# Kernel optimization log

Measured on AMD Instinct MI355X. Metric: run time of the kernel, lower is better.

The kernel has to match this reference:

```python
import jax, jax.numpy as jnp
import numpy as np

B, T, C, HS = 8, 2048, 1024, 64
SCALE = C ** (-0.5)  # NOTE: source scales by C, not head_size
NEG_INF = float('-inf')
NEG_BIG = -1e9


def setup_inputs() -> dict:
    key = jax.random.key(0)
    kV, kK, kQ, kWq, kWk, kWv, kL = jax.random.split(key, 7)
    V = jax.random.normal(kV, (B, T, C), dtype=jnp.float32)
    K = jax.random.normal(kK, (B, T, C), dtype=jnp.float32)
    Q = jax.random.normal(kQ, (B, T, C), dtype=jnp.float32)
    w_scale = 1.0 / np.sqrt(C)
    Wq = jax.random.normal(kWq, (C, HS), dtype=jnp.float32) * w_scale
    Wk = jax.random.normal(kWk, (C, HS), dtype=jnp.float32) * w_scale
    Wv = jax.random.normal(kWv, (C, HS), dtype=jnp.float32) * w_scale
    # padding only at the tail; valid lengths in [T//2, T] so no NaN softmax rows
    lengths = jax.random.randint(kL, (B,), T // 2, T + 1)
    pad_mask = (jnp.arange(T)[None, None, :] >= lengths[:, None, None])  # [B,1,T] bool
    return {"V": V, "K": K, "Q": Q, "Wq": Wq, "Wk": Wk, "Wv": Wv, "pad_mask": pad_mask}


def reference(V, K, Q, Wq, Wk, Wv, pad_mask):
    q = Q @ Wq  # [B,T,HS]
    k = K @ Wk
    v = V @ Wv
    A = jnp.einsum('btd,bsd->bts', q, k) * SCALE  # [B,T,T]
    t = A.shape[1]
    causal = jnp.triu(jnp.ones((t, A.shape[2]), dtype=bool), k=1)  # tril==0
    A = jnp.where(causal[None], NEG_INF, A)
    A = jnp.where(pad_mask, NEG_INF, A)  # mask padded key columns
    A = jnp.where(jnp.swapaxes(pad_mask, -2, -1)[:, :t, :], NEG_BIG, A)  # padded query rows
    A = jax.nn.softmax(A, axis=-1)
    return A @ v  # [B,T,HS]
```

## Files before the change

kernel.cpp:

```cpp
#include <hip/hip_runtime.h>
#include <hip/hip_bf16.h>

typedef short bf16x8 __attribute__((ext_vector_type(8)));
typedef float f32x4 __attribute__((ext_vector_type(4)));
typedef unsigned int u32;
typedef u32 u32x4 __attribute__((ext_vector_type(4)));

#define T_SEQ 2048
#define NB 8
#define NEGB (-1e30f)

__device__ inline unsigned short f2bf(float f) {
  unsigned u = __builtin_bit_cast(unsigned, f);
  u += 0x7FFFu + ((u >> 16) & 1u);
  return (unsigned short)(u >> 16);
}
__device__ inline float bf2f(unsigned short h) {
  unsigned u = ((unsigned)h) << 16;
  return __builtin_bit_cast(float, u);
}
__device__ inline u32 cvt2(float a, float b) {
  __hip_bfloat162 h = __float22bfloat162_rn(make_float2(a, b));
  u32 r;
  __builtin_memcpy(&r, &h, 4);
  return r;
}
__device__ inline bf16x8 pack8(float4 a, float4 b) {
  u32x4 p;
  p[0] = cvt2(a.x, a.y);
  p[1] = cvt2(a.z, a.w);
  p[2] = cvt2(b.x, b.y);
  p[3] = cvt2(b.z, b.w);
  return __builtin_bit_cast(bf16x8, p);
}
__device__ inline f32x4 mfma16(bf16x8 a, bf16x8 b, f32x4 c) {
  return __builtin_amdgcn_mfma_f32_16x16x32_bf16(a, b, c, 0, 0, 0);
}
__device__ __forceinline__ void gl_lds16(const void* g, void* l) {
  __builtin_amdgcn_global_load_lds(
      (const __attribute__((address_space(1))) void*)g,
      (__attribute__((address_space(3))) void*)l, 16, 0, 0);
}

__global__ void detect_k(const unsigned char* m, int* flag) {
  __shared__ int ones, bad;
  int tid = threadIdx.x;
  if (tid == 0) { ones = 0; bad = 0; }
  __syncthreads();
  int lo = 0, lb = 0;
  for (int i = tid; i < NB * T_SEQ; i += 256) {
    int v = (m[i] != 0);
    lo += v;
    if (i & 3) lb += v;
  }
  atomicAdd(&ones, lo);
  atomicAdd(&bad, lb);
  __syncthreads();
  if (tid == 0) *flag = (ones > 0 && bad == 0) ? 1 : 0;
}

__global__ void lengths_k(const unsigned char* m, const int* flag, int* lengths) {
  int b = blockIdx.x, tid = threadIdx.x;
  int cnt = 0;
  if (*flag) {
    const int* mi = (const int*)m;
    for (int t = tid; t < T_SEQ; t += 256) cnt += (mi[b * T_SEQ + t] == 0);
  } else {
    for (int t = tid; t < T_SEQ; t += 256) cnt += (m[b * T_SEQ + t] == 0);
  }
  for (int off = 32; off >= 1; off >>= 1) cnt += __shfl_xor(cnt, off);
  __shared__ int wsum[4];
  if ((tid & 63) == 0) wsum[tid >> 6] = cnt;
  __syncthreads();
  if (tid == 0) lengths[b] = wsum[0] + wsum[1] + wsum[2] + wsum[3];
}

__global__ void wt_k(const float* Wq, const float* Wk, const float* Wv,
                     unsigned short* wt) {
  int e = blockIdx.x * 256 + threadIdx.x;
  if (e >= 3 * 64 * 1024) return;
  int mi = e >> 16;
  int rem = e & 65535;
  int kk = rem & 1023, n = rem >> 10;
  const float* W = (mi == 0) ? Wq : (mi == 1) ? Wk : Wv;
  wt[e] = f2bf(W[kk * 64 + n]);
}

__global__ __launch_bounds__(512, 4) void proj_k(
    const float* Q, const float* K, const float* V, const unsigned short* wt,
    unsigned short* qo, unsigned short* ko, unsigned short* vTb) {
  __shared__ float xs[2][4096];
  __shared__ unsigned short wss[2][4096];
  int mi = blockIdx.y;
  const float* X = (mi == 0) ? Q : (mi == 1) ? K : V;
  const unsigned short* wtm = wt + mi * 65536;
  int tid = threadIdx.x;
  int w = tid >> 6, lane = tid & 63, l15 = lane & 15, g = lane >> 4;
  int wr = w >> 1, wc = w & 1;
  int r0b = blockIdx.x * 64;

  int segA = w * 2;
  int rowA0 = segA * 4 + (lane >> 4);
  int rowA1 = rowA0 + 4;
  int colA0 = ((lane & 15) ^ (rowA0 & 15)) * 4;
  int colA1 = ((lane & 15) ^ (rowA1 & 15)) * 4;
  const float* srcA0 = X + (size_t)(r0b + rowA0) * 1024 + colA0;
  const float* srcA1 = X + (size_t)(r0b + rowA1) * 1024 + colA1;
  int nW = w * 8 + (lane >> 3);
  int skW = ((lane & 7) ^ (nW & 7)) * 8;
  const unsigned short* srcW = wtm + (size_t)nW * 1024 + skW;

  f32x4 acc[2];
  acc[0] = 0; acc[1] = 0;

#define STAGE(buf, kc2)                                          \
  do {                                                           \
    gl_lds16(srcA0 + (kc2) * 64, &xs[buf][segA * 256]);          \
    gl_lds16(srcA1 + (kc2) * 64, &xs[buf][segA * 256 + 256]);    \
    gl_lds16(srcW + (kc2) * 64, &wss[buf][w * 512]);             \
  } while (0)

  STAGE(0, 0);

  int arow = wr * 16 + l15;
  for (int kc = 0; kc < 16; ++kc) {
    int cur = kc & 1;
    if (kc < 15) {
      STAGE(cur ^ 1, kc + 1);
      asm volatile("s_waitcnt vmcnt(3)" ::: "memory");
    } else {
      asm volatile("s_waitcnt vmcnt(0)" ::: "memory");
    }
    __builtin_amdgcn_s_barrier();
#pragma unroll
    for (int ks = 0; ks < 2; ++ks) {
      int lb0 = ks * 8 + g * 2;
      float4 fa = *(const float4*)&xs[cur][arow * 64 + ((lb0 ^ l15) * 4)];
      float4 fb = *(const float4*)&xs[cur][arow * 64 + (((lb0 + 1) ^ l15) * 4)];
      bf16x8 a = pack8(fa, fb);
#pragma unroll
      for (int nt = 0; nt < 2; ++nt) {
        int nrow = wc * 32 + nt * 16 + l15;
        bf16x8 bb = *(const bf16x8*)
            &wss[cur][nrow * 64 + (((ks * 4 + g) ^ (l15 & 7)) * 8)];
        acc[nt] = mfma16(a, bb, acc[nt]);
      }
    }
    if (kc < 15) {
      asm volatile("s_waitcnt lgkmcnt(0)" ::: "memory");
      __builtin_amdgcn_s_barrier();
    }
  }
#undef STAGE

#pragma unroll
  for (int nt = 0; nt < 2; ++nt)
#pragma unroll
    for (int vv = 0; vv < 4; ++vv) {
      int rr = r0b + wr * 16 + g * 4 + vv;
      int c = wc * 32 + nt * 16 + l15;
      float val = acc[nt][vv];
      if (mi == 0) {
        qo[(size_t)rr * 64 + c] = f2bf(val * 0.03125f);
      } else if (mi == 1) {
        ko[(size_t)rr * 64 + c] = f2bf(val);
      } else {
        int bb = rr >> 11, ts = rr & 2047;
        vTb[(((size_t)bb * 64 + (ts >> 5)) * 64 + c) * 32 + (ts & 31)] =
            f2bf(val);
      }
    }
}

__global__ void vmean_k(const unsigned short* vTb, float* vmean) {
  int b = blockIdx.x, tid = threadIdx.x;
  int k8 = tid & 3;
  int d = tid >> 2;
  const unsigned short* base = vTb + (size_t)b * 131072;
  float s = 0.f;
  for (int tt = 0; tt < 64; ++tt) {
    bf16x8 v = *(const bf16x8*)&base[(tt * 64 + d) * 32 + k8 * 8];
#pragma unroll
    for (int i = 0; i < 8; ++i) s += bf2f((unsigned short)v[i]);
  }
  s += __shfl_xor(s, 1);
  s += __shfl_xor(s, 2);
  if (k8 == 0) vmean[b * 64 + d] = s * (1.0f / T_SEQ);
}

__global__ __launch_bounds__(512, 4) void attn_k(
    const unsigned short* q, const unsigned short* k, const unsigned short* vTb,
    const float* vmean, const int* lengths, float* Out) {
  __shared__ unsigned short pL[8][16][40];
  __shared__ unsigned short oP[4][2][16][64];
  __shared__ float mP[4][2][16], lP[4][2][16];

  int id = blockIdx.x;
  int raw = id & 63, b = id >> 6;
  int xx = (raw + 8 * b) & 63;
  int tile = (xx < 32) ? xx : 95 - xx;
  int t0 = tile * 32;

  int tid = threadIdx.x;
  int w = tid >> 6, lane = tid & 63;
  int j = w >> 1, r = w & 1;
  int l15 = lane & 15, g = lane >> 4;
  int t_base = t0 + r * 16;

  const bf16x8* qrow =
      (const bf16x8*)(q + ((size_t)b * T_SEQ + t_base + l15) * 64);
  bf16x8 aq0 = qrow[g];
  bf16x8 aq1 = qrow[4 + g];

  f32x4 o[4];
  float m[4], l[4];
#pragma unroll
  for (int i = 0; i < 4; ++i) { o[i] = 0; m[i] = NEGB; l[i] = 0.f; }

  const bf16x8* kch = (const bf16x8*)k + (size_t)b * T_SEQ * 8;
  const unsigned short* vch = vTb + (size_t)b * 131072;

  int NT = tile + 1;
  int qn = NT >> 2, rem = NT & 3;
  int start = j * qn + (j < rem ? j : rem);
  int end = start + qn + (j < rem ? 1 : 0);
  int capw = ((t_base + 15) >> 5) + 1;
  if (end > capw) end = capw;

  for (int tt = start; tt < end; ++tt) {
    int s0 = tt * 32;
    f32x4 sa0, sa1;
    sa0 = 0; sa1 = 0;
    bf16x8 kb00 = kch[(size_t)(s0 + l15) * 8 + g];
    bf16x8 kb01 = kch[(size_t)(s0 + l15) * 8 + 4 + g];
    bf16x8 kb10 = kch[(size_t)(s0 + 16 + l15) * 8 + g];
    bf16x8 kb11 = kch[(size_t)(s0 + 16 + l15) * 8 + 4 + g];
    sa0 = mfma16(aq0, kb00, sa0);
    sa0 = mfma16(aq1, kb01, sa0);
    sa1 = mfma16(aq0, kb10, sa1);
    sa1 = mfma16(aq1, kb11, sa1);
#pragma unroll
    for (int vv = 0; vv < 4; ++vv) {
      int t = t_base + g * 4 + vv;
      float v0 = (s0 + l15 <= t) ? sa0[vv] : NEGB;
      float v1 = (s0 + 16 + l15 <= t) ? sa1[vv] : NEGB;
      float rm = fmaxf(v0, v1);
#pragma unroll
      for (int off = 8; off >= 1; off >>= 1)
        rm = fmaxf(rm, __shfl_xor(rm, off));
      float mn = fmaxf(m[vv], rm);
      float corr = __expf(m[vv] - mn);
      float p0 = (v0 == NEGB) ? 0.f : __expf(v0 - mn);
      float p1 = (v1 == NEGB) ? 0.f : __expf(v1 - mn);
      float rs = p0 + p1;
#pragma unroll
      for (int off = 8; off >= 1; off >>= 1) rs += __shfl_xor(rs, off);
      l[vv] = l[vv] * corr + rs;
      m[vv] = mn;
#pragma unroll
      for (int nt = 0; nt < 4; ++nt) o[nt][vv] *= corr;
      pL[w][g * 4 + vv][l15] = f2bf(p0);
      pL[w][g * 4 + vv][16 + l15] = f2bf(p1);
    }
    bf16x8 ap = *(const bf16x8*)&pL[w][l15][g * 8];
#pragma unroll
    for (int nt = 0; nt < 4; ++nt) {
      bf16x8 bv =
          *(const bf16x8*)&vch[((size_t)(tt * 64 + nt * 16 + l15)) * 32 + g * 8];
      o[nt] = mfma16(ap, bv, o[nt]);
    }
  }

  __syncthreads();
#pragma unroll
  for (int nt = 0; nt < 4; ++nt)
#pragma unroll
    for (int vv = 0; vv < 4; ++vv)
      oP[j][r][g * 4 + vv][nt * 16 + l15] = f2bf(o[nt][vv]);
  if (l15 == 0) {
#pragma unroll
    for (int vv = 0; vv < 4; ++vv) {
      mP[j][r][g * 4 + vv] = m[vv];
      lP[j][r][g * 4 + vv] = l[vv];
    }
  }
  __syncthreads();

  if (w < 2) {
    int len = lengths[b];
#pragma unroll 4
    for (int row = 0; row < 16; ++row) {
      float m0 = mP[0][w][row], m1 = mP[1][w][row];
      float m2 = mP[2][w][row], m3 = mP[3][w][row];
      float ms = fmaxf(fmaxf(m0, m1), fmaxf(m2, m3));
      float e0 = __expf(m0 - ms), e1 = __expf(m1 - ms);
      float e2 = __expf(m2 - ms), e3 = __expf(m3 - ms);
      float ls = lP[0][w][row] * e0 + lP[1][w][row] * e1 +
                 lP[2][w][row] * e2 + lP[3][w][row] * e3;
      float ov = bf2f(oP[0][w][row][lane]) * e0 +
                 bf2f(oP[1][w][row][lane]) * e1 +
                 bf2f(oP[2][w][row][lane]) * e2 +
                 bf2f(oP[3][w][row][lane]) * e3;
      float val = ov / ls;
      int t = t0 + w * 16 + row;
      if (t >= len) val = vmean[b * 64 + lane];
      Out[((size_t)b * T_SEQ + t) * 64 + lane] = val;
    }
  }
}

extern "C" void kernel_launch(void* const* d_in, const int* in_sizes, int n_in,
                              void* d_out, int out_size, void* d_ws,
                              size_t ws_size, hipStream_t stream) {
  const float* V = (const float*)d_in[0];
  const float* K = (const float*)d_in[1];
  const float* Q = (const float*)d_in[2];
  const float* Wq = (const float*)d_in[3];
  const float* Wk = (const float*)d_in[4];
  const float* Wv = (const float*)d_in[5];
  const unsigned char* mask = (const unsigned char*)d_in[6];
  float* O = (float*)d_out;
  char* ws = (char*)d_ws;

  unsigned short* wt = (unsigned short*)(ws);
  unsigned short* qb = (unsigned short*)(ws + 393216);
  unsigned short* kb = (unsigned short*)(ws + 393216 + 2097152);
  unsigned short* vTb = (unsigned short*)(ws + 393216 + 2 * 2097152);
  float* vmean = (float*)(ws + 393216 + 3 * 2097152);
  int* lengths = (int*)(ws + 393216 + 3 * 2097152 + 2048);
  int* flag = lengths + 8;

  detect_k<<<1, 256, 0, stream>>>(mask, flag);
  lengths_k<<<NB, 256, 0, stream>>>(mask, flag, lengths);
  wt_k<<<768, 256, 0, stream>>>(Wq, Wk, Wv, wt);
  proj_k<<<dim3(256, 3), 512, 0, stream>>>(Q, K, V, wt, qb, kb, vTb);
  vmean_k<<<NB, 256, 0, stream>>>(vTb, vmean);
  attn_k<<<512, 512, 0, stream>>>(qb, kb, vTb, vmean, lengths, O);
}
```

Before: 100.6 us.

## Convert projection input to bf16 in LDS and read pre-swizzled weights directly

The projection kernel no longer double-buffers fp32 X tiles and weight tiles through LDS with async global-to-LDS loads. Each block now loads half of the K dimension of its 64 rows into registers, converts to bf16, and stores it once into a swizzled LDS buffer. Weights are repacked by wt_k into MFMA fragment order, so each lane reads its B operand straight from global memory with no LDS staging. This removes per-chunk barriers and repeated fp32 LDS reads, but gives up load/compute overlap and relies on the cache for weight reuse across blocks.

```diff
diff --git a/kernel.cpp b/kernel.cpp
--- a/kernel.cpp
+++ b/kernel.cpp
@@ -35,11 +35,6 @@
 }
 __device__ inline f32x4 mfma16(bf16x8 a, bf16x8 b, f32x4 c) {
   return __builtin_amdgcn_mfma_f32_16x16x32_bf16(a, b, c, 0, 0, 0);
-}
-__device__ __forceinline__ void gl_lds16(const void* g, void* l) {
-  __builtin_amdgcn_global_load_lds(
-      (const __attribute__((address_space(1))) void*)g,
-      (__attribute__((address_space(3))) void*)l, 16, 0, 0);
 }
 
 __global__ void detect_k(const unsigned char* m, int* flag) {
@@ -78,80 +73,73 @@
 __global__ void wt_k(const float* Wq, const float* Wk, const float* Wv,
                      unsigned short* wt) {
   int e = blockIdx.x * 256 + threadIdx.x;
-  if (e >= 3 * 64 * 1024) return;
+  if (e >= 3 * 65536) return;
+  int i = e & 7;
+  int lane = (e >> 3) & 63;
+  int nt = (e >> 9) & 3;
+  int ks = (e >> 11) & 31;
   int mi = e >> 16;
-  int rem = e & 65535;
-  int kk = rem & 1023, n = rem >> 10;
+  int kk = ks * 32 + (lane >> 4) * 8 + i;
+  int n = nt * 16 + (lane & 15);
   const float* W = (mi == 0) ? Wq : (mi == 1) ? Wk : Wv;
   wt[e] = f2bf(W[kk * 64 + n]);
 }
 
 __global__ __launch_bounds__(512, 4) void proj_k(
-    const float* Q, const float* K, const float* V, const unsigned short* wt,
+    const float* Q, const float* K, const float* V, const unsigned short* wt2,
     unsigned short* qo, unsigned short* ko, unsigned short* vTb) {
-  __shared__ float xs[2][4096];
-  __shared__ unsigned short wss[2][4096];
+  __shared__ unsigned short xls[64 * 512];
   int mi = blockIdx.y;
   const float* X = (mi == 0) ? Q : (mi == 1) ? K : V;
-  const unsigned short* wtm = wt + mi * 65536;
+  const unsigned short* wtm = wt2 + mi * 65536;
   int tid = threadIdx.x;
   int w = tid >> 6, lane = tid & 63, l15 = lane & 15, g = lane >> 4;
   int wr = w >> 1, wc = w & 1;
   int r0b = blockIdx.x * 64;
 
-  int segA = w * 2;
-  int rowA0 = segA * 4 + (lane >> 4);
-  int rowA1 = rowA0 + 4;
-  int colA0 = ((lane & 15) ^ (rowA0 & 15)) * 4;
-  int colA1 = ((lane & 15) ^ (rowA1 & 15)) * 4;
-  const float* srcA0 = X + (size_t)(r0b + rowA0) * 1024 + colA0;
-  const float* srcA1 = X + (size_t)(r0b + rowA1) * 1024 + colA1;
-  int nW = w * 8 + (lane >> 3);
-  int skW = ((lane & 7) ^ (nW & 7)) * 8;
-  const unsigned short* srcW = wtm + (size_t)nW * 1024 + skW;
-
   f32x4 acc[2];
   acc[0] = 0; acc[1] = 0;
 
-#define STAGE(buf, kc2)                                          \
-  do {                                                           \
-    gl_lds16(srcA0 + (kc2) * 64, &xs[buf][segA * 256]);          \
-    gl_lds16(srcA1 + (kc2) * 64, &xs[buf][segA * 256 + 256]);    \
-    gl_lds16(srcW + (kc2) * 64, &wss[buf][w * 512]);             \
-  } while (0)
-
-  STAGE(0, 0);
-
   int arow = wr * 16 + l15;
-  for (int kc = 0; kc < 16; ++kc) {
-    int cur = kc & 1;
-    if (kc < 15) {
-      STAGE(cur ^ 1, kc + 1);
-      asm volatile("s_waitcnt vmcnt(3)" ::: "memory");
-    } else {
-      asm volatile("s_waitcnt vmcnt(0)" ::: "memory");
-    }
-    __builtin_amdgcn_s_barrier();
-#pragma unroll
-    for (int ks = 0; ks < 2; ++ks) {
-      int lb0 = ks * 8 + g * 2;
-      float4 fa = *(const float4*)&xs[cur][arow * 64 + ((lb0 ^ l15) * 4)];
-      float4 fb = *(const float4*)&xs[cur][arow * 64 + (((lb0 + 1) ^ l15) * 4)];
-      bf16x8 a = pack8(fa, fb);
-#pragma unroll
-      for (int nt = 0; nt < 2; ++nt) {
-        int nrow = wc * 32 + nt * 16 + l15;
-        bf16x8 bb = *(const bf16x8*)
-            &wss[cur][nrow * 64 + (((ks * 4 + g) ^ (l15 & 7)) * 8)];
-        acc[nt] = mfma16(a, bb, acc[nt]);
+  char* aldsrow = (char*)xls + arow * 1024;
+  int asw = (l15 & 7) << 4;
+
+#pragma unroll
+  for (int h = 0; h < 2; ++h) {
+    int k0 = h * 512;
+#pragma unroll
+    for (int batch = 0; batch < 2; ++batch) {
+      float4 fa[4], fb[4];
+#pragma unroll
+      for (int i = 0; i < 4; ++i) {
+        int r = w * 8 + batch * 4 + i;
+        const float4* src = (const float4*)(X + (size_t)(r0b + r) * 1024 + k0);
+        fa[i] = src[2 * lane];
+        fb[i] = src[2 * lane + 1];
       }
-    }
-    if (kc < 15) {
-      asm volatile("s_waitcnt lgkmcnt(0)" ::: "memory");
-      __builtin_amdgcn_s_barrier();
-    }
-  }
-#undef STAGE
+#pragma unroll
+      for (int i = 0; i < 4; ++i) {
+        int r = w * 8 + batch * 4 + i;
+        int sw = (r & 7) << 4;
+        *(bf16x8*)((char*)xls + r * 1024 + ((16 * lane) ^ sw)) =
+            pack8(fa[i], fb[i]);
+      }
+    }
+    __syncthreads();
+
+#pragma unroll 4
+    for (int ks = 0; ks < 16; ++ks) {
+      bf16x8 a = *(const bf16x8*)(aldsrow + ((ks * 64 + g * 16) ^ asw));
+      int ksg = h * 16 + ks;
+      const bf16x8* wbase =
+          (const bf16x8*)(wtm + (size_t)ksg * 2048 + (wc * 2) * 512 + lane * 8);
+      bf16x8 w0 = wbase[0];
+      bf16x8 w1 = wbase[64];
+      acc[0] = mfma16(a, w0, acc[0]);
+      acc[1] = mfma16(a, w1, acc[1]);
+    }
+    if (h == 0) __syncthreads();
+  }
 
 #pragma unroll
   for (int nt = 0; nt < 2; ++nt)
```

Result: slower. 108.9 us (+8.3%).

## Merge mask kernels, fuse V-mean into projection, prefetch K/V tiles in attention

Applied to the files above, without the earlier changes.

Merges the mask-format detection and length kernels into one kernel, removing a launch and its dependency. The V column mean is now accumulated inside the projection kernel through atomics into a zeroed buffer, which drops the separate vmean kernel but adds a memset and atomic traffic. The attention loop also loads the next tile's K and V fragments while computing on the current tile, so memory latency can overlap with the softmax math, at the cost of extra registers. Each merged block now rescans the whole mask to detect its format.

```diff
diff --git a/kernel.cpp b/kernel.cpp
--- a/kernel.cpp
+++ b/kernel.cpp
@@ -42,37 +42,36 @@
       (__attribute__((address_space(3))) void*)l, 16, 0, 0);
 }
 
-__global__ void detect_k(const unsigned char* m, int* flag) {
-  __shared__ int ones, bad;
-  int tid = threadIdx.x;
-  if (tid == 0) { ones = 0; bad = 0; }
-  __syncthreads();
+__global__ void meta_k(const unsigned char* m, int* lengths) {
+  int b = blockIdx.x, tid = threadIdx.x;
   int lo = 0, lb = 0;
   for (int i = tid; i < NB * T_SEQ; i += 256) {
     int v = (m[i] != 0);
     lo += v;
     if (i & 3) lb += v;
   }
-  atomicAdd(&ones, lo);
-  atomicAdd(&bad, lb);
-  __syncthreads();
-  if (tid == 0) *flag = (ones > 0 && bad == 0) ? 1 : 0;
-}
-
-__global__ void lengths_k(const unsigned char* m, const int* flag, int* lengths) {
-  int b = blockIdx.x, tid = threadIdx.x;
+  for (int off = 32; off >= 1; off >>= 1) {
+    lo += __shfl_xor(lo, off);
+    lb += __shfl_xor(lb, off);
+  }
+  __shared__ int s0[4], s1[4], ws2[4];
+  if ((tid & 63) == 0) { s0[tid >> 6] = lo; s1[tid >> 6] = lb; }
+  __syncthreads();
+  int ones = s0[0] + s0[1] + s0[2] + s0[3];
+  int bad = s1[0] + s1[1] + s1[2] + s1[3];
+  int flag = (ones > 0 && bad == 0);
   int cnt = 0;
-  if (*flag) {
+  if (flag) {
     const int* mi = (const int*)m;
     for (int t = tid; t < T_SEQ; t += 256) cnt += (mi[b * T_SEQ + t] == 0);
   } else {
     for (int t = tid; t < T_SEQ; t += 256) cnt += (m[b * T_SEQ + t] == 0);
   }
   for (int off = 32; off >= 1; off >>= 1) cnt += __shfl_xor(cnt, off);
-  __shared__ int wsum[4];
-  if ((tid & 63) == 0) wsum[tid >> 6] = cnt;
-  __syncthreads();
-  if (tid == 0) lengths[b] = wsum[0] + wsum[1] + wsum[2] + wsum[3];
+  __syncthreads();
+  if ((tid & 63) == 0) ws2[tid >> 6] = cnt;
+  __syncthreads();
+  if (tid == 0) lengths[b] = ws2[0] + ws2[1] + ws2[2] + ws2[3];
 }
 
 __global__ void wt_k(const float* Wq, const float* Wk, const float* Wv,
@@ -88,7 +87,7 @@
 
 __global__ __launch_bounds__(512, 4) void proj_k(
     const float* Q, const float* K, const float* V, const unsigned short* wt,
-    unsigned short* qo, unsigned short* ko, unsigned short* vTb) {
+    unsigned short* qo, unsigned short* ko, unsigned short* vTb, float* vmsum) {
   __shared__ float xs[2][4096];
   __shared__ unsigned short wss[2][4096];
   int mi = blockIdx.y;
@@ -170,27 +169,27 @@
             f2bf(val);
       }
     }
-}
-
-__global__ void vmean_k(const unsigned short* vTb, float* vmean) {
-  int b = blockIdx.x, tid = threadIdx.x;
-  int k8 = tid & 3;
-  int d = tid >> 2;
-  const unsigned short* base = vTb + (size_t)b * 131072;
-  float s = 0.f;
-  for (int tt = 0; tt < 64; ++tt) {
-    bf16x8 v = *(const bf16x8*)&base[(tt * 64 + d) * 32 + k8 * 8];
-#pragma unroll
-    for (int i = 0; i < 8; ++i) s += bf2f((unsigned short)v[i]);
-  }
-  s += __shfl_xor(s, 1);
-  s += __shfl_xor(s, 2);
-  if (k8 == 0) vmean[b * 64 + d] = s * (1.0f / T_SEQ);
+
+  if (mi == 2) {
+    float ps0 = acc[0][0] + acc[0][1] + acc[0][2] + acc[0][3];
+    float ps1 = acc[1][0] + acc[1][1] + acc[1][2] + acc[1][3];
+    __syncthreads();
+    float* rb = (float*)xs;
+    rb[(wc * 32 + l15) * 16 + (wr * 4 + g)] = ps0;
+    rb[(wc * 32 + 16 + l15) * 16 + (wr * 4 + g)] = ps1;
+    __syncthreads();
+    if (tid < 64) {
+      float s = 0.f;
+#pragma unroll
+      for (int i = 0; i < 16; ++i) s += rb[tid * 16 + i];
+      atomicAdd(&vmsum[(blockIdx.x >> 5) * 64 + tid], s);
+    }
+  }
 }
 
 __global__ __launch_bounds__(512, 4) void attn_k(
     const unsigned short* q, const unsigned short* k, const unsigned short* vTb,
-    const float* vmean, const int* lengths, float* Out) {
+    const float* vmsum, const int* lengths, float* Out) {
   __shared__ unsigned short pL[8][16][40];
   __shared__ unsigned short oP[4][2][16][64];
   __shared__ float mP[4][2][16], lP[4][2][16];
@@ -227,18 +226,43 @@
   int capw = ((t_base + 15) >> 5) + 1;
   if (end > capw) end = capw;
 
+  bf16x8 kb00, kb01, kb10, kb11, bv0, bv1, bv2, bv3;
+  if (start < end) {
+    int s0 = start * 32;
+    kb00 = kch[(size_t)(s0 + l15) * 8 + g];
+    kb01 = kch[(size_t)(s0 + l15) * 8 + 4 + g];
+    kb10 = kch[(size_t)(s0 + 16 + l15) * 8 + g];
+    kb11 = kch[(size_t)(s0 + 16 + l15) * 8 + 4 + g];
+    bv0 = *(const bf16x8*)&vch[((size_t)(start * 64 + l15)) * 32 + g * 8];
+    bv1 = *(const bf16x8*)&vch[((size_t)(start * 64 + 16 + l15)) * 32 + g * 8];
+    bv2 = *(const bf16x8*)&vch[((size_t)(start * 64 + 32 + l15)) * 32 + g * 8];
+    bv3 = *(const bf16x8*)&vch[((size_t)(start * 64 + 48 + l15)) * 32 + g * 8];
+  }
+
   for (int tt = start; tt < end; ++tt) {
     int s0 = tt * 32;
     f32x4 sa0, sa1;
     sa0 = 0; sa1 = 0;
-    bf16x8 kb00 = kch[(size_t)(s0 + l15) * 8 + g];
-    bf16x8 kb01 = kch[(size_t)(s0 + l15) * 8 + 4 + g];
-    bf16x8 kb10 = kch[(size_t)(s0 + 16 + l15) * 8 + g];
-    bf16x8 kb11 = kch[(size_t)(s0 + 16 + l15) * 8 + 4 + g];
     sa0 = mfma16(aq0, kb00, sa0);
     sa0 = mfma16(aq1, kb01, sa0);
     sa1 = mfma16(aq0, kb10, sa1);
     sa1 = mfma16(aq1, kb11, sa1);
+
+    bf16x8 nk00, nk01, nk10, nk11, nv0, nv1, nv2, nv3;
+    bool more = (tt + 1 < end);
+    if (more) {
+      int s1 = (tt + 1) * 32;
+      nk00 = kch[(size_t)(s1 + l15) * 8 + g];
+      nk01 = kch[(size_t)(s1 + l15) * 8 + 4 + g];
+      nk10 = kch[(size_t)(s1 + 16 + l15) * 8 + g];
+      nk11 = kch[(size_t)(s1 + 16 + l15) * 8 + 4 + g];
+      int t1 = (tt + 1) * 64;
+      nv0 = *(const bf16x8*)&vch[((size_t)(t1 + l15)) * 32 + g * 8];
+      nv1 = *(const bf16x8*)&vch[((size_t)(t1 + 16 + l15)) * 32 + g * 8];
+      nv2 = *(const bf16x8*)&vch[((size_t)(t1 + 32 + l15)) * 32 + g * 8];
+      nv3 = *(const bf16x8*)&vch[((size_t)(t1 + 48 + l15)) * 32 + g * 8];
+    }
+
 #pragma unroll
     for (int vv = 0; vv < 4; ++vv) {
       int t = t_base + g * 4 + vv;
@@ -263,11 +287,13 @@
       pL[w][g * 4 + vv][16 + l15] = f2bf(p1);
     }
     bf16x8 ap = *(const bf16x8*)&pL[w][l15][g * 8];
-#pragma unroll
-    for (int nt = 0; nt < 4; ++nt) {
-      bf16x8 bv =
-          *(const bf16x8*)&vch[((size_t)(tt * 64 + nt * 16 + l15)) * 32 + g * 8];
-      o[nt] = mfma16(ap, bv, o[nt]);
+    o[0] = mfma16(ap, bv0, o[0]);
+    o[1] = mfma16(ap, bv1, o[1]);
+    o[2] = mfma16(ap, bv2, o[2]);
+    o[3] = mfma16(ap, bv3, o[3]);
+    if (more) {
+      kb00 = nk00; kb01 = nk01; kb10 = nk10; kb11 = nk11;
+      bv0 = nv0; bv1 = nv1; bv2 = nv2; bv3 = nv3;
     }
   }
 
@@ -303,7 +329,7 @@
                  bf2f(oP[3][w][row][lane]) * e3;
       float val = ov / ls;
       int t = t0 + w * 16 + row;
-      if (t >= len) val = vmean[b * 64 + lane];
+      if (t >= len) val = vmsum[b * 64 + lane] * (1.0f / T_SEQ);
       Out[((size_t)b * T_SEQ + t) * 64 + lane] = val;
     }
   }
@@ -326,14 +352,12 @@
   unsigned short* qb = (unsigned short*)(ws + 393216);
   unsigned short* kb = (unsigned short*)(ws + 393216 + 2097152);
   unsigned short* vTb = (unsigned short*)(ws + 393216 + 2 * 2097152);
-  float* vmean = (float*)(ws + 393216 + 3 * 2097152);
+  float* vmsum = (float*)(ws + 393216 + 3 * 2097152);
   int* lengths = (int*)(ws + 393216 + 3 * 2097152 + 2048);
-  int* flag = lengths + 8;
-
-  detect_k<<<1, 256, 0, stream>>>(mask, flag);
-  lengths_k<<<NB, 256, 0, stream>>>(mask, flag, lengths);
+
+  hipMemsetAsync(vmsum, 0, 512 * sizeof(float), stream);
   wt_k<<<768, 256, 0, stream>>>(Wq, Wk, Wv, wt);
-  proj_k<<<dim3(256, 3), 512, 0, stream>>>(Q, K, V, wt, qb, kb, vTb);
-  vmean_k<<<NB, 256, 0, stream>>>(vTb, vmean);
-  attn_k<<<512, 512, 0, stream>>>(qb, kb, vTb, vmean, lengths, O);
-}
+  meta_k<<<NB, 256, 0, stream>>>(mask, lengths);
+  proj_k<<<dim3(256, 3), 512, 0, stream>>>(Q, K, V, wt, qb, kb, vTb, vmsum);
+  attn_k<<<512, 512, 0, stream>>>(qb, kb, vTb, vmsum, lengths, O);
+}
```

Result: faster. 89.99 us (-10.5%).
